# Performance work log

Hardware: AMD Instinct MI355X
Metric: run time of the kernel (lower is better)

## Reference

```python
import jax, jax.numpy as jnp
import numpy as np

D_MODEL = 1024
D_FF = 4096
NUM_EXPERTS = 8
TOP_K = 2
TEMPERATURE = 1.0


def setup_inputs() -> dict:
    key = jax.random.key(0)
    ks = jax.random.split(key, 5)
    hidden_states = jax.random.normal(ks[0], (4, 2048, D_MODEL), dtype=jnp.float32)
    # Router gate: nn.Linear(d_model, num_experts, bias=False), weight [E, d], std=0.01
    gate_w = jax.random.normal(ks[1], (NUM_EXPERTS, D_MODEL), dtype=jnp.float32) * 0.01
    # Expert FFN weights: torch Linear weight is [out, in]; init std=0.02, biases zero
    w1 = jax.random.normal(ks[2], (NUM_EXPERTS, D_FF, D_MODEL), dtype=jnp.float32) * 0.02
    b1 = jnp.zeros((NUM_EXPERTS, D_FF), dtype=jnp.float32)
    w2 = jax.random.normal(ks[3], (NUM_EXPERTS, D_MODEL, D_FF), dtype=jnp.float32) * 0.02
    b2 = jnp.zeros((NUM_EXPERTS, D_MODEL), dtype=jnp.float32)
    return {"hidden_states": hidden_states, "gate_w": gate_w,
            "w1": w1, "b1": b1, "w2": w2, "b2": b2}


def reference(hidden_states, gate_w, w1, b1, w2, b2):
    B, S, D = hidden_states.shape
    E, K = NUM_EXPERTS, TOP_K
    x = hidden_states.reshape(-1, D)  # [T, d]
    T = x.shape[0]

    # --- Router (fp32, eval mode: no noise) ---
    logits = jnp.einsum('td,ed->te', x, gate_w) / TEMPERATURE  # [T, E]
    probs = jax.nn.softmax(logits, axis=-1)
    top_vals, top_idx = jax.lax.top_k(probs, K)               # [T, K]
    weights = top_vals / jnp.sum(top_vals, axis=-1, keepdims=True)

    # Dense combine weights per expert: [T, E]
    one_hot = jax.nn.one_hot(top_idx, E, dtype=x.dtype)        # [T, K, E]
    combine = jnp.einsum('tke,tk->te', one_hot, weights)       # [T, E]

    # --- Load-balancing aux loss ---
    importance = jnp.mean(probs, axis=0)                       # [E]
    load = jnp.sum(one_hot, axis=(0, 1)) / (T * K)             # [E]
    aux_loss = E * jnp.sum(importance * load)

    # --- Expert dispatch/combine (loop over fixed small E) ---
    out = jnp.zeros_like(x)
    for e in range(E):
        h = jax.nn.gelu(x @ w1[e].T + b1[e], approximate=False)  # [T, d_ff]
        y = h @ w2[e].T + b2[e]                                   # [T, d]
        out = out + combine[:, e:e + 1] * y

    return out.reshape(B, S, D), aux_loss
```

## Files before the change

kernel.cpp:

```cpp
#include <hip/hip_runtime.h>
#include <cstdint>
#include <math.h>

#define T_TOK 8192
#define DM 1024
#define DFF 4096
#define NE 8
#define WLMAX 72

typedef __attribute__((ext_vector_type(8))) short short8;
typedef __attribute__((ext_vector_type(4))) float f32x4;

#define GLDS16(g, l) __builtin_amdgcn_global_load_lds( \
    (const __attribute__((address_space(1))) void*)(g), \
    (__attribute__((address_space(3))) void*)(l), 16, 0, 0)

static __device__ __forceinline__ unsigned short f2bf(float f) {
    union { float f; unsigned int u; } v; v.f = f;
    unsigned int r = (v.u + 0x7FFFu + ((v.u >> 16) & 1u)) >> 16;
    return (unsigned short)r;
}

static __device__ __forceinline__ float gelu_f(float v) {
    float z = fabsf(v) * 0.70710678118654752f;
    float t = 1.f / (1.f + 0.3275911f * z);
    float p = t * (0.254829592f + t * (-0.284496736f + t * (1.421413741f +
              t * (-1.453152027f + t * 1.061405429f))));
    float erfz = 1.f - p * __expf(-z * z);
    float s = (v >= 0.f) ? erfz : -erfz;
    return 0.5f * v * (1.f + s);
}

__global__ __launch_bounds__(256) void conv_flat(const float* __restrict__ src,
                                                 unsigned short* __restrict__ dst,
                                                 long long n)
{
    long long i = ((long long)blockIdx.x * 256 + threadIdx.x) * 4;
    if (i >= n) return;
    const float4 v = *(const float4*)(src + i);
    uint2 u;
    u.x = (unsigned)f2bf(v.x) | ((unsigned)f2bf(v.y) << 16);
    u.y = (unsigned)f2bf(v.z) | ((unsigned)f2bf(v.w) << 16);
    *(uint2*)(dst + i) = u;
}

__global__ __launch_bounds__(256) void conv_rows(const float* __restrict__ src,
                                                 unsigned short* __restrict__ dst,
                                                 long long src_off, long long src_stride,
                                                 int ncols)
{
    long long row = blockIdx.y;
    int c = (blockIdx.x * 256 + threadIdx.x) * 4;
    if (c >= ncols) return;
    const float4 v = *(const float4*)(src + src_off + row * src_stride + c);
    uint2 u;
    u.x = (unsigned)f2bf(v.x) | ((unsigned)f2bf(v.y) << 16);
    u.y = (unsigned)f2bf(v.z) | ((unsigned)f2bf(v.w) << 16);
    *(uint2*)(dst + row * (long long)ncols + c) = u;
}

__global__ __launch_bounds__(256) void router_kernel(
    const float* __restrict__ x, const float* __restrict__ gw,
    int* __restrict__ counts, float* __restrict__ imp,
    int* __restrict__ ptok, float* __restrict__ pw)
{
    __shared__ float4 sgw[NE * 256];
    __shared__ float simp[NE];
    const int tid = threadIdx.x;
    #pragma unroll
    for (int j = 0; j < 8; ++j) sgw[tid + j * 256] = ((const float4*)gw)[tid + j * 256];
    if (tid < NE) simp[tid] = 0.f;
    __syncthreads();

    const int wid = tid >> 6, lane = tid & 63;
    const int t = blockIdx.x * 4 + wid;
    float acc[NE];
    #pragma unroll
    for (int e = 0; e < NE; ++e) acc[e] = 0.f;
    const float4* xr = (const float4*)(x + (size_t)t * DM);
    #pragma unroll
    for (int j = 0; j < 4; ++j) {
        int idx = lane + j * 64;
        float4 xv = xr[idx];
        #pragma unroll
        for (int e = 0; e < NE; ++e) {
            float4 g = sgw[e * 256 + idx];
            acc[e] += xv.x * g.x + xv.y * g.y + xv.z * g.z + xv.w * g.w;
        }
    }
    #pragma unroll
    for (int off = 32; off; off >>= 1) {
        #pragma unroll
        for (int e = 0; e < NE; ++e) acc[e] += __shfl_xor(acc[e], off);
    }
    if (lane == 0) {
        float m = acc[0];
        #pragma unroll
        for (int e = 1; e < NE; ++e) m = fmaxf(m, acc[e]);
        float p[NE], s = 0.f;
        #pragma unroll
        for (int e = 0; e < NE; ++e) { p[e] = expf(acc[e] - m); s += p[e]; }
        float inv = 1.f / s;
        #pragma unroll
        for (int e = 0; e < NE; ++e) { p[e] *= inv; atomicAdd(&simp[e], p[e]); }
        int i0 = 0;
        #pragma unroll
        for (int e = 1; e < NE; ++e) if (p[e] > p[i0]) i0 = e;
        int i1 = (i0 == 0) ? 1 : 0;
        #pragma unroll
        for (int e = 0; e < NE; ++e) if (e != i0 && p[e] > p[i1]) i1 = e;
        float v0 = p[i0], v1 = p[i1], wsum = v0 + v1;
        int s0 = atomicAdd(&counts[i0], 1);
        ptok[i0 * T_TOK + s0] = t; pw[i0 * T_TOK + s0] = v0 / wsum;
        int s1 = atomicAdd(&counts[i1], 1);
        ptok[i1 * T_TOK + s1] = t; pw[i1 * T_TOK + s1] = v1 / wsum;
    }
    __syncthreads();
    if (tid < NE) atomicAdd(&imp[tid], simp[tid]);
}

__global__ void finalize_kernel(const int* __restrict__ counts,
                                const float* __restrict__ imp,
                                int* __restrict__ offs, int* __restrict__ wl,
                                float* __restrict__ aux_out)
{
    if (threadIdx.x == 0 && blockIdx.x == 0) {
        int o = 0; float aux = 0.f;
        for (int e = 0; e < NE; ++e) {
            offs[e] = o; o += counts[e];
            aux += (imp[e] / (float)T_TOK) * ((float)counts[e] / (float)(T_TOK * 2));
        }
        offs[NE] = o;
        int it = 0;
        for (int e = 0; e < NE; ++e) {
            int mts = (counts[e] + 255) >> 8;
            for (int mt = 0; mt < mts; ++mt) wl[it++] = (e << 16) | mt;
        }
        for (; it < WLMAX; ++it) wl[it] = -1;
        *aux_out = (float)NE * aux;
    }
}

__global__ __launch_bounds__(256) void pregather_kernel(
    const float* __restrict__ x, const int* __restrict__ counts,
    const int* __restrict__ offs, const int* __restrict__ ptok,
    unsigned short* __restrict__ xg, int* __restrict__ tc, int* __restrict__ tokpair)
{
    const int e = blockIdx.y;
    const int slot = blockIdx.x * 4 + (threadIdx.x >> 6);
    if (slot >= counts[e]) return;
    const int tok = ptok[e * T_TOK + slot];
    const int lane = threadIdx.x & 63;
    const int p = offs[e] + slot;
    if (lane == 0) {
        int k = atomicAdd(&tc[tok], 1);
        tokpair[tok * 2 + k] = p;
    }
    const float4* src = (const float4*)(x + (size_t)tok * DM);
    uint2* dst = (uint2*)(xg + (size_t)p * DM);
    #pragma unroll
    for (int j = 0; j < 4; ++j) {
        float4 v = src[lane + j * 64];
        uint2 u;
        u.x = (unsigned)f2bf(v.x) | ((unsigned)f2bf(v.y) << 16);
        u.y = (unsigned)f2bf(v.z) | ((unsigned)f2bf(v.w) << 16);
        dst[lane + j * 64] = u;
    }
}

__global__ __launch_bounds__(256) void combine_kernel(
    const float* __restrict__ yv, const int* __restrict__ tokpair,
    float* __restrict__ out)
{
    const int t = blockIdx.x;
    const int c = threadIdx.x;
    const long long p0 = tokpair[t * 2], p1 = tokpair[t * 2 + 1];
    const float4 a = ((const float4*)(yv + p0 * DM))[c];
    const float4 b = ((const float4*)(yv + p1 * DM))[c];
    float4 o;
    o.x = a.x + b.x; o.y = a.y + b.y; o.z = a.z + b.z; o.w = a.w + b.w;
    ((float4*)(out + (long long)t * DM))[c] = o;
}

template<int EPI>
__global__ __launch_bounds__(512, 2) void gemm_bt(
    const unsigned short* __restrict__ A,
    const unsigned short* __restrict__ W,
    const float* __restrict__ bias,
    const int* __restrict__ counts, const int* __restrict__ offs,
    const int* __restrict__ ptok, const float* __restrict__ pw,
    const int* __restrict__ wl,
    unsigned short* __restrict__ Hout, float* __restrict__ yv,
    int FFC, int cch, int wfull)
{
    const int bx = blockIdx.x;
    const int item = wl[(bx & 7) * 9 + (bx >> 3)];
    if (item < 0) return;
    const int e = item >> 16, mt = item & 0xffff;
    const int n_e = counts[e];
    int rows_here = n_e - mt * 256; if (rows_here > 256) rows_here = 256;
    const long long row_lo = (long long)offs[e] + (long long)mt * 256;
    const int nt = blockIdx.y;
    const int KD = (EPI == 0) ? DM : FFC;

    __shared__ unsigned short lA[3][256 * 32];
    __shared__ unsigned short lB[3][256 * 32];

    const int tid = threadIdx.x, lane = tid & 63, wid = tid >> 6;
    const int wr = wid >> 2, wc = wid & 3;
    const int hi = lane >> 4, lo = lane & 15;

    int wrow0; long long wstride, wcol0;
    if (EPI == 0) {
        wrow0 = e * (wfull ? DFF : FFC) + (wfull ? cch * FFC : 0) + nt * 256;
        wstride = DM; wcol0 = 0;
    } else {
        wrow0 = e * DM + nt * 256;
        wstride = (wfull ? DFF : FFC); wcol0 = (wfull ? (long long)cch * FFC : 0);
    }

    const unsigned short* aaddr[2];
    const unsigned short* baddr[2];
    #pragma unroll
    for (int j = 0; j < 2; ++j) {
        int li = tid + j * 512;
        int r = li >> 2;
        int sg = ((li & 3) ^ ((r >> 1) & 3)) * 8;
        int rc = (r < rows_here) ? r : (rows_here - 1);
        aaddr[j] = A + (row_lo + rc) * KD + sg;
        baddr[j] = W + (long long)(wrow0 + r) * wstride + wcol0 + sg;
    }

    int offA[8], offB[4];
    #pragma unroll
    for (int mi = 0; mi < 8; ++mi) {
        int row = wr * 128 + mi * 16 + lo;
        offA[mi] = row * 32 + ((hi ^ ((row >> 1) & 3)) * 8);
    }
    #pragma unroll
    for (int nj = 0; nj < 4; ++nj) {
        int row = wc * 64 + nj * 16 + lo;
        offB[nj] = row * 32 + ((hi ^ ((row >> 1) & 3)) * 8);
    }

    f32x4 acc[8][4];
    #pragma unroll
    for (int i = 0; i < 8; ++i)
        #pragma unroll
        for (int j = 0; j < 4; ++j) acc[i][j] = (f32x4)0.f;

#define STAGE(buf, t) do { \
        const long long _k0 = (long long)(t) * 32; \
        GLDS16(aaddr[0] + _k0, &lA[buf][tid * 8]); \
        GLDS16(aaddr[1] + _k0, &lA[buf][(tid + 512) * 8]); \
        GLDS16(baddr[0] + _k0, &lB[buf][tid * 8]); \
        GLDS16(baddr[1] + _k0, &lB[buf][(tid + 512) * 8]); \
    } while (0)

    const int NT = KD >> 5;

    STAGE(0, 0);
    STAGE(1, 1);
    asm volatile("s_waitcnt vmcnt(4)" ::: "memory");
    __builtin_amdgcn_s_barrier();

    for (int t = 0; t < NT; ++t) {
        const int cb = t % 3;
        if (t + 2 < NT) STAGE((t + 2) % 3, t + 2);
        short8 af[8], bf[4];
        #pragma unroll
        for (int mi = 0; mi < 8; ++mi) af[mi] = *(const short8*)(&lA[cb][offA[mi]]);
        #pragma unroll
        for (int nj = 0; nj < 4; ++nj) bf[nj] = *(const short8*)(&lB[cb][offB[nj]]);
        #pragma unroll
        for (int mi = 0; mi < 8; ++mi)
            #pragma unroll
            for (int nj = 0; nj < 4; ++nj)
                acc[mi][nj] = __builtin_amdgcn_mfma_f32_16x16x32_bf16(af[mi], bf[nj], acc[mi][nj], 0, 0, 0);
        if (t + 2 < NT) { asm volatile("s_waitcnt vmcnt(4)" ::: "memory"); }
        else            { asm volatile("s_waitcnt vmcnt(0)" ::: "memory"); }
        __builtin_amdgcn_s_barrier();
    }

    const int rbase = hi * 4;
    if (EPI == 0) {
        #pragma unroll
        for (int mi = 0; mi < 8; ++mi) {
            #pragma unroll
            for (int r = 0; r < 4; ++r) {
                int m = wr * 128 + mi * 16 + rbase + r;
                if (m >= rows_here) continue;
                long long hrow = (row_lo + m) * FFC;
                #pragma unroll
                for (int nj = 0; nj < 4; ++nj) {
                    int f = nt * 256 + wc * 64 + nj * 16 + lo;
                    float v = acc[mi][nj][r] + bias[e * DFF + cch * FFC + f];
                    Hout[hrow + f] = f2bf(gelu_f(v));
                }
            }
        }
    } else {
        #pragma unroll
        for (int mi = 0; mi < 8; ++mi) {
            #pragma unroll
            for (int r = 0; r < 4; ++r) {
                int m = wr * 128 + mi * 16 + rbase + r;
                if (m >= rows_here) continue;
                int pidx = e * T_TOK + mt * 256 + m;
                float wgt = pw[pidx];
                float* yrow = yv + (row_lo + m) * DM;
                #pragma unroll
                for (int nj = 0; nj < 4; ++nj) {
                    int d = nt * 256 + wc * 64 + nj * 16 + lo;
                    float v = acc[mi][nj][r];
                    if (cch == 0) yrow[d] = wgt * (v + bias[e * DM + d]);
                    else          yrow[d] += wgt * v;
                }
            }
        }
    }
#undef STAGE
}

extern "C" void kernel_launch(void* const* d_in, const int* in_sizes, int n_in,
                              void* d_out, int out_size, void* d_ws, size_t ws_size,
                              hipStream_t stream)
{
    const float* x  = (const float*)d_in[0];
    const float* gw = (const float*)d_in[1];
    const float* w1 = (const float*)d_in[2];
    const float* b1 = (const float*)d_in[3];
    const float* w2 = (const float*)d_in[4];
    const float* b2 = (const float*)d_in[5];
    float* out = (float*)d_out;

    char* ws = (char*)d_ws;
    int*   counts  = (int*)ws;
    float* imp     = (float*)(ws + 64);
    int*   offs    = (int*)(ws + 128);
    int*   tc      = (int*)(ws + 256);
    int*   wl      = (int*)(ws + 33024);
    int*   tokpair = (int*)(ws + 33792);
    int*   ptok    = (int*)(ws + 99840);
    float* pw      = (float*)(ws + 99840 + (size_t)NE * T_TOK * 4);
    size_t cur = 99840 + (size_t)NE * T_TOK * 8;
    cur = (cur + 511) & ~(size_t)511;

    unsigned short* xg = (unsigned short*)(ws + cur);
    cur += (size_t)2 * T_TOK * DM * 2;
    cur = (cur + 511) & ~(size_t)511;
    float* yv = (float*)(ws + cur);
    cur += (size_t)2 * T_TOK * DM * 4;

    const size_t wfull_bytes = (size_t)NE * DFF * DM * 2;
    const size_t hrow_total  = 2 * (size_t)T_TOK;

    int FFC = 0, wfull = 0;
    unsigned short *w1b = nullptr, *w2b = nullptr, *H = nullptr;
    for (int f = DFF; f >= 256; f >>= 1) {
        size_t need = cur + 2 * wfull_bytes + hrow_total * (size_t)f * 2;
        if (need <= ws_size) { FFC = f; wfull = 1; break; }
    }
    if (wfull) {
        w1b = (unsigned short*)(ws + cur); cur += wfull_bytes;
        w2b = (unsigned short*)(ws + cur); cur += wfull_bytes;
        H   = (unsigned short*)(ws + cur);
    } else {
        for (int f = 2048; f >= 256; f >>= 1) {
            size_t wc = (size_t)NE * f * DM * 2;
            size_t need = cur + 2 * wc + hrow_total * (size_t)f * 2;
            if (need <= ws_size) { FFC = f; break; }
        }
        if (FFC == 0) return;
        size_t wc = (size_t)NE * FFC * DM * 2;
        w1b = (unsigned short*)(ws + cur); cur += wc;
        w2b = (unsigned short*)(ws + cur); cur += wc;
        H   = (unsigned short*)(ws + cur);
    }

    hipMemsetAsync(ws, 0, 33024, stream);

    router_kernel<<<T_TOK / 4, 256, 0, stream>>>(x, gw, counts, imp, ptok, pw);
    finalize_kernel<<<1, 64, 0, stream>>>(counts, imp, offs, wl, out + (size_t)out_size - 1);
    {
        dim3 gp(T_TOK / 4, NE);
        pregather_kernel<<<gp, 256, 0, stream>>>(x, counts, offs, ptok, xg, tc, tokpair);
    }
    if (wfull) {
        long long n = (long long)NE * DFF * DM;
        conv_flat<<<(unsigned)(n / 1024), 256, 0, stream>>>(w1, w1b, n);
        conv_flat<<<(unsigned)(n / 1024), 256, 0, stream>>>(w2, w2b, n);
    }

    const int NCH = DFF / FFC;
    for (int c = 0; c < NCH; ++c) {
        if (!wfull) {
            dim3 gc1((unsigned)((long long)FFC * DM / 1024), NE);
            conv_rows<<<gc1, 256, 0, stream>>>(w1, w1b,
                (long long)c * FFC * DM, (long long)DFF * DM, FFC * DM);
            dim3 gc2((unsigned)((FFC + 1023) / 1024), NE * DM);
            conv_rows<<<gc2, 256, 0, stream>>>(w2, w2b,
                (long long)c * FFC, (long long)DFF, FFC);
        }
        dim3 g1(WLMAX, FFC / 256, 1);
        gemm_bt<0><<<g1, 512, 0, stream>>>(xg, w1b, b1, counts, offs, ptok, pw, wl, H, yv, FFC, c, wfull);
        dim3 g2(WLMAX, DM / 256, 1);
        gemm_bt<1><<<g2, 512, 0, stream>>>(H, w2b, b2, counts, offs, ptok, pw, wl, H, yv, FFC, c, wfull);
    }
    combine_kernel<<<T_TOK, 256, 0, stream>>>(yv, tokpair, out);
}
```

Measured before the change: 978.2 us.

## Restructure GEMM main loop into 4-phase ping-pong schedule with interleaved loads

```diff
diff --git a/kernel.cpp b/kernel.cpp
--- a/kernel.cpp
+++ b/kernel.cpp
@@ -202,13 +202,14 @@
     const long long row_lo = (long long)offs[e] + (long long)mt * 256;
     const int nt = blockIdx.y;
     const int KD = (EPI == 0) ? DM : FFC;
-
-    __shared__ unsigned short lA[3][256 * 32];
-    __shared__ unsigned short lB[3][256 * 32];
+    const int NT = KD >> 6;
+
+    __shared__ unsigned short lA[2 * 2 * 256 * 32];
+    __shared__ unsigned short lB[2 * 2 * 256 * 32];
 
     const int tid = threadIdx.x, lane = tid & 63, wid = tid >> 6;
     const int wr = wid >> 2, wc = wid & 3;
-    const int hi = lane >> 4, lo = lane & 15;
+    const int lo = lane & 15, hi = lane >> 4;
 
     int wrow0; long long wstride, wcol0;
     if (EPI == 0) {
@@ -249,37 +250,79 @@
         #pragma unroll
         for (int j = 0; j < 4; ++j) acc[i][j] = (f32x4)0.f;
 
-#define STAGE(buf, t) do { \
-        const long long _k0 = (long long)(t) * 32; \
-        GLDS16(aaddr[0] + _k0, &lA[buf][tid * 8]); \
-        GLDS16(aaddr[1] + _k0, &lA[buf][(tid + 512) * 8]); \
-        GLDS16(baddr[0] + _k0, &lB[buf][tid * 8]); \
-        GLDS16(baddr[1] + _k0, &lB[buf][(tid + 512) * 8]); \
+#define STG(LDSA, ADDR, tile, k) do { \
+        const int _b = (((tile) & 1) * 2 + (k)) * 8192; \
+        const long long _ko = (long long)(tile) * 64 + (k) * 32; \
+        GLDS16((ADDR)[0] + _ko, &LDSA[_b + tid * 8]); \
+        GLDS16((ADDR)[1] + _ko, &LDSA[_b + (tid + 512) * 8]); \
     } while (0)
 
-    const int NT = KD >> 5;
-
-    STAGE(0, 0);
-    STAGE(1, 1);
-    asm volatile("s_waitcnt vmcnt(4)" ::: "memory");
+#define MFMA_CL(g, BF0, BF1) do { \
+        __builtin_amdgcn_s_setprio(1); \
+        _Pragma("unroll") \
+        for (int mi = 0; mi < 8; ++mi) { \
+            acc[mi][2 * (g)]     = __builtin_amdgcn_mfma_f32_16x16x32_bf16(af[mi], BF0, acc[mi][2 * (g)], 0, 0, 0); \
+            acc[mi][2 * (g) + 1] = __builtin_amdgcn_mfma_f32_16x16x32_bf16(af[mi], BF1, acc[mi][2 * (g) + 1], 0, 0, 0); \
+        } \
+        __builtin_amdgcn_s_setprio(0); \
+    } while (0)
+
+    STG(lA, aaddr, 0, 0); STG(lB, baddr, 0, 0);
+    STG(lA, aaddr, 0, 1); STG(lB, baddr, 0, 1);
+    STG(lA, aaddr, 1, 0); STG(lB, baddr, 1, 0);
+    STG(lA, aaddr, 1, 1);
+    asm volatile("s_waitcnt vmcnt(6)" ::: "memory");
     __builtin_amdgcn_s_barrier();
-
-    for (int t = 0; t < NT; ++t) {
-        const int cb = t % 3;
-        if (t + 2 < NT) STAGE((t + 2) % 3, t + 2);
-        short8 af[8], bf[4];
-        #pragma unroll
-        for (int mi = 0; mi < 8; ++mi) af[mi] = *(const short8*)(&lA[cb][offA[mi]]);
-        #pragma unroll
-        for (int nj = 0; nj < 4; ++nj) bf[nj] = *(const short8*)(&lB[cb][offB[nj]]);
-        #pragma unroll
-        for (int mi = 0; mi < 8; ++mi)
+    asm volatile("" ::: "memory");
+
+    short8 af[8];
+
+    for (int kt = 0; kt < NT; ++kt) {
+        const int bA0 = ((kt & 1) * 2 + 0) * 8192;
+        const int bA1 = ((kt & 1) * 2 + 1) * 8192;
+
+        {
             #pragma unroll
-            for (int nj = 0; nj < 4; ++nj)
-                acc[mi][nj] = __builtin_amdgcn_mfma_f32_16x16x32_bf16(af[mi], bf[nj], acc[mi][nj], 0, 0, 0);
-        if (t + 2 < NT) { asm volatile("s_waitcnt vmcnt(4)" ::: "memory"); }
-        else            { asm volatile("s_waitcnt vmcnt(0)" ::: "memory"); }
-        __builtin_amdgcn_s_barrier();
+            for (int mi = 0; mi < 8; ++mi) af[mi] = *(const short8*)(&lA[bA0 + offA[mi]]);
+            short8 bf0 = *(const short8*)(&lB[bA0 + offB[0]]);
+            short8 bf1 = *(const short8*)(&lB[bA0 + offB[1]]);
+            if (kt + 1 < NT) STG(lB, baddr, kt + 1, 1);
+            asm volatile("" ::: "memory"); __builtin_amdgcn_s_barrier();
+            asm volatile("s_waitcnt lgkmcnt(0)" ::: "memory");
+            MFMA_CL(0, bf0, bf1);
+            asm volatile("" ::: "memory"); __builtin_amdgcn_s_barrier(); asm volatile("" ::: "memory");
+        }
+        {
+            short8 bf2 = *(const short8*)(&lB[bA0 + offB[2]]);
+            short8 bf3 = *(const short8*)(&lB[bA0 + offB[3]]);
+            if (kt + 2 < NT) STG(lA, aaddr, kt + 2, 0);
+            asm volatile("" ::: "memory"); __builtin_amdgcn_s_barrier();
+            asm volatile("s_waitcnt lgkmcnt(0)" ::: "memory");
+            MFMA_CL(1, bf2, bf3);
+            asm volatile("" ::: "memory"); __builtin_amdgcn_s_barrier(); asm volatile("" ::: "memory");
+        }
+        {
+            #pragma unroll
+            for (int mi = 0; mi < 8; ++mi) af[mi] = *(const short8*)(&lA[bA1 + offA[mi]]);
+            short8 bf0 = *(const short8*)(&lB[bA1 + offB[0]]);
+            short8 bf1 = *(const short8*)(&lB[bA1 + offB[1]]);
+            if (kt + 2 < NT) STG(lB, baddr, kt + 2, 0);
+            asm volatile("" ::: "memory"); __builtin_amdgcn_s_barrier();
+            asm volatile("s_waitcnt lgkmcnt(0)" ::: "memory");
+            MFMA_CL(0, bf0, bf1);
+            asm volatile("" ::: "memory"); __builtin_amdgcn_s_barrier(); asm volatile("" ::: "memory");
+        }
+        {
+            short8 bf2 = *(const short8*)(&lB[bA1 + offB[2]]);
+            short8 bf3 = *(const short8*)(&lB[bA1 + offB[3]]);
+            if (kt + 2 < NT) STG(lA, aaddr, kt + 2, 1);
+            asm volatile("" ::: "memory"); __builtin_amdgcn_s_barrier();
+            asm volatile("s_waitcnt lgkmcnt(0)" ::: "memory");
+            MFMA_CL(1, bf2, bf3);
+            if (kt + 2 < NT) { asm volatile("s_waitcnt vmcnt(6)" ::: "memory"); }
+            else             { asm volatile("s_waitcnt vmcnt(0)" ::: "memory"); }
+            asm volatile("" ::: "memory"); __builtin_amdgcn_s_barrier(); asm volatile("" ::: "memory");
+        }
     }
 
     const int rbase = hi * 4;
@@ -319,7 +362,8 @@
             }
         }
     }
-#undef STAGE
+#undef STG
+#undef MFMA_CL
 }
 
 extern "C" void kernel_launch(void* const* d_in, const int* in_sizes, int n_in,
```

New measurement: 836.2 us. 14.5% less time.
